# Optimization experiments

Hardware: AMD Instinct MI355X
Metric: run time of the kernel (lower is better)

Reference implementation:

```python
import jax, jax.numpy as jnp
import numpy as np

N, C, H, K = 4096, 512, 128, 3
NEG = -jnp.inf


def _linear(x, W, b):
    return x @ W.T + b


def _lrelu(x):
    return jnp.where(x > 0, x, 0.01 * x)  # nn.LeakyReLU default slope


def _cos_sim(x, y):
    # torch cal_cos_similarity: xy / (|x| |y|^T), NaN (0/0) -> 0
    xy = x @ y.T
    den = jnp.linalg.norm(x, axis=1, keepdims=True) * jnp.linalg.norm(y, axis=1, keepdims=True).T
    return xy / jnp.where(den == 0, 1.0, den)


def setup_inputs() -> dict:
    key = jax.random.key(0)
    ks = jax.random.split(key, 24)
    x_hidden = jax.random.normal(ks[0], (N, H), jnp.float32)
    cm = (jax.random.uniform(ks[1], (N, C)) < 0.05).astype(jnp.float32)
    # ensure every concept has at least one member stock (no empty concepts)
    cm = cm.at[jnp.arange(C) % N, jnp.arange(C)].set(1.0)
    market_value = jax.random.uniform(ks[2], (N,), jnp.float32, 0.1, 1.0)
    s = 1.0 / np.sqrt(H)
    inp = {"x_hidden": x_hidden, "concept_matrix": cm, "market_value": market_value}
    names = ["ps", "ps_fore", "ps_back", "hs", "hs_fore", "hs_back", "indi"]
    for i, n in enumerate(names):
        inp[f"W_{n}"] = jax.random.uniform(ks[3 + 2 * i], (H, H), jnp.float32, -s, s)
        inp[f"b_{n}"] = jax.random.uniform(ks[4 + 2 * i], (H,), jnp.float32, -s, s)
    inp["W_out"] = jax.random.uniform(ks[20], (1, H), jnp.float32, -s, s)
    inp["b_out"] = jax.random.uniform(ks[21], (1,), jnp.float32, -s, s)
    return inp


def reference(x_hidden, concept_matrix, market_value,
              W_ps, b_ps, W_ps_fore, b_ps_fore, W_ps_back, b_ps_back,
              W_hs, b_hs, W_hs_fore, b_hs_fore, W_hs_back, b_hs_back,
              W_indi, b_indi, W_out, b_out):
    x = x_hidden
    n = x.shape[0]
    # --- predefined-concept (ps) branch ---
    s2c = concept_matrix * market_value[:, None]                     # [N,C]
    s2c_den = s2c.sum(0)[None, :] * concept_matrix + 1.0
    s2c = s2c / s2c_den
    hidden = s2c.T @ x                                               # [C,H]
    valid1 = hidden.sum(1) != 0                                      # row-filter mask
    s2c2 = jax.nn.softmax(x @ hidden.T, axis=0)                      # softmax over stocks
    hidden = (s2c2.T @ x) * valid1[:, None]                          # [C,H]
    c2s = jax.nn.softmax(jnp.where(valid1[None, :], _cos_sim(x, hidden), NEG), axis=1)
    p_shared = _linear(c2s @ hidden, W_ps, b_ps)
    p_back = _linear(p_shared, W_ps_back, b_ps_back)
    out_ps = _lrelu(_linear(p_shared, W_ps_fore, b_ps_fore))
    # --- hidden-concept (hs) branch ---
    h = x - p_back
    hs2c = _cos_sim(h, h)                                            # [N,N]
    diag = jnp.diagonal(hs2c)
    hs2c = hs2c * (1.0 - jnp.eye(n, dtype=h.dtype))
    idx = jax.lax.top_k(hs2c, K)[1]                                  # [N,K]
    mask = jnp.zeros((n, n), h.dtype).at[jnp.arange(n)[:, None], idx].set(1.0)
    hs2c = hs2c * mask
    hs2c = hs2c + jnp.diag((hs2c.sum(0) != 0).astype(h.dtype) * diag)
    hidden2 = hs2c.T @ h                                             # [N,H]
    valid2 = hidden2.sum(1) != 0
    hidden2 = hidden2 * valid2[:, None]
    hc2s = jax.nn.softmax(jnp.where(valid2[None, :], _cos_sim(h, hidden2), NEG), axis=1)
    h_shared = _linear(hc2s @ hidden2, W_hs, b_hs)
    h_back = _linear(h_shared, W_hs_back, b_hs_back)
    out_hs = _lrelu(_linear(h_shared, W_hs_fore, b_hs_fore))
    # --- individual branch ---
    indiv = x - p_back - h_back
    out_indi = _lrelu(_linear(indiv, W_indi, b_indi))
    all_info = out_ps + out_hs + out_indi
    return _linear(all_info, W_out, b_out).squeeze()                 # [N]
```

## Files before the change

kernel.cpp:

```cpp
#include <hip/hip_runtime.h>
#include <hip/hip_fp16.h>
#include <math.h>

#define N 4096
#define C 512
#define H 128
#define PAD 40
#define WP 136
#define FWP 136
#define SP 136

typedef __attribute__((ext_vector_type(8))) short bf16x8;
typedef __attribute__((ext_vector_type(4))) float f32x4;


__device__ inline float wave_reduce_sum(float v) {
#pragma unroll
  for (int m = 32; m; m >>= 1) v += __shfl_xor(v, m);
  return v;
}

__device__ inline float lrelu(float v) { return v > 0.f ? v : 0.01f * v; }

__device__ inline bool better(float v, int j, float w, int k) {
// ... 94 lines not shown
               (unsigned)ll[12] | ((unsigned)ll[13] << 16), (unsigned)ll[14] | ((unsigned)ll[15] << 16)};
  *(uint4*)&thi[off] = ph0; *(uint4*)&thi[off + 8] = ph1;
  *(uint4*)&tlo[off] = pl0; *(uint4*)&tlo[off + 8] = pl1;
}


__global__ __launch_bounds__(64) void k_colsum_s2c(
    const float* __restrict__ cm, const float* __restrict__ mv,
    float* __restrict__ colsum_c) {
  int c = blockIdx.x * 64 + threadIdx.x;
  int i0 = blockIdx.y * 256;
  float acc = 0.f;
  for (int i = i0; i < i0 + 256; i++) acc += cm[(size_t)i * C + c] * mv[i];
  atomicAdd(&colsum_c[c], acc);
}

__global__ __launch_bounds__(256) void k_colstats(const float* __restrict__ sc,
                                                  float* __restrict__ colmax,
                                                  float* __restrict__ colsum) {
  __shared__ float red[256];
  int c = blockIdx.x, t = threadIdx.x;
  float v[16];
  float m = -3e38f;
#pragma unroll
  for (int q = 0; q < 16; q++) {
    v[q] = sc[(size_t)(q * 256 + t) * C + c];
    m = fmaxf(m, v[q]);
  }
  red[t] = m; __syncthreads();
  for (int s = 128; s; s >>= 1) { if (t < s) red[t] = fmaxf(red[t], red[t + s]); __syncthreads(); }
  m = red[0]; __syncthreads();
  float sum = 0.f;
#pragma unroll
  for (int q = 0; q < 16; q++) sum += __expf(v[q] - m);
  red[t] = sum; __syncthreads();
  for (int s = 128; s; s >>= 1) { if (t < s) red[t] += red[t + s]; __syncthreads(); }
  if (t == 0) { colmax[c] = m; colsum[c] = red[0]; }
}

__global__ __launch_bounds__(256) void k_cs_softmax(
    const float* __restrict__ sc, const float* __restrict__ xnorm,
    const float* __restrict__ hnorm, const float* __restrict__ valid1,
    unsigned short* __restrict__ cshi, unsigned short* __restrict__ cslo) {
  __shared__ float red[256];
  int i = blockIdx.x, t = threadIdx.x;
  float xn = xnorm[i];
  float r0 = sc[(size_t)i * C + t], r1 = sc[(size_t)i * C + 256 + t];
  float d0 = xn * hnorm[t], d1 = xn * hnorm[256 + t];
  float c0 = r0 / (d0 == 0.f ? 1.f : d0);
  float c1 = r1 / (d1 == 0.f ? 1.f : d1);
  float s0 = (valid1[t] != 0.f) ? c0 : -3e38f;
  float s1 = (valid1[256 + t] != 0.f) ? c1 : -3e38f;
  red[t] = fmaxf(s0, s1); __syncthreads();
  for (int s = 128; s; s >>= 1) { if (t < s) red[t] = fmaxf(red[t], red[t + s]); __syncthreads(); }
  float m = red[0]; __syncthreads();
  float p0 = (s0 > -1e37f) ? __expf(s0 - m) : 0.f;
  float p1 = (s1 > -1e37f) ? __expf(s1 - m) : 0.f;
  red[t] = p0 + p1; __syncthreads();
  for (int s = 128; s; s >>= 1) { if (t < s) red[t] += red[t + s]; __syncthreads(); }
  float inv = 1.f / red[0];
  float a = p0 * inv, b = p1 * inv;
  unsigned short ha = f2bf(a), hb = f2bf(b);
  cshi[(size_t)i * C + t] = ha;
  cslo[(size_t)i * C + t] = f2bf(a - bf2f(ha));
  cshi[(size_t)i * C + 256 + t] = hb;
  cslo[(size_t)i * C + 256 + t] = f2bf(b - bf2f(hb));
}

__global__ __launch_bounds__(64) void k_fin_hidden2(
    const float* __restrict__ h, const float* __restrict__ diagv,
    const float* __restrict__ colsum_m, float* __restrict__ hidden2,
    unsigned short* __restrict__ h2hi, unsigned short* __restrict__ h2lo,
    float* __restrict__ valid2f) {
  int j = blockIdx.x, t = threadIdx.x;
  float add = (colsum_m[j] != 0.f) ? diagv[j] : 0.f;
  float a = hidden2[(size_t)j * H + t] + add * h[(size_t)j * H + t];
  float b = hidden2[(size_t)j * H + 64 + t] + add * h[(size_t)j * H + 64 + t];
  float s = a + b, ss = a * a + b * b;
#pragma unroll
  for (int m = 32; m; m >>= 1) { s += __shfl_xor(s, m); ss += __shfl_xor(ss, m); }
  bool valid = (s != 0.f);
  a = valid ? a : 0.f; b = valid ? b : 0.f;
  hidden2[(size_t)j * H + t] = a;
  hidden2[(size_t)j * H + 64 + t] = b;
  float inv = (valid && ss > 0.f) ? (1.f / sqrtf(ss)) : 1.f;
  float va = a * inv, vb = b * inv;
  unsigned short ha = f2bf(va), hb = f2bf(vb);
  h2hi[(size_t)j * H + t] = ha;
  h2lo[(size_t)j * H + t] = f2bf(va - bf2f(ha));
  h2hi[(size_t)j * H + 64 + t] = hb;
  h2lo[(size_t)j * H + 64 + t] = f2bf(vb - bf2f(hb));
  if (t == 0) valid2f[j] = valid ? 1.f : 0.f;
}

__global__ __launch_bounds__(256) void k_mfma_nt(
    const unsigned short* __restrict__ Ahi, const unsigned short* __restrict__ Alo,
    const unsigned short* __restrict__ Bhi, const unsigned short* __restrict__ Blo,
    float* __restrict__ out, int Nn) {
  __shared__ __align__(16) unsigned short sAh[64 * PAD];
  __shared__ __align__(16) unsigned short sAl[64 * PAD];
  __shared__ __align__(16) unsigned short sBh[128 * PAD];
  __shared__ __align__(16) unsigned short sBl[128 * PAD];
  int tid = threadIdx.x;
  int bm = blockIdx.y * 64, bn = blockIdx.x * 128;
  int lane = tid & 63, w = tid >> 6;
  int wm = (w & 1) * 32, wn = (w >> 1) * 64;
  int l15 = lane & 15, quad = lane >> 4;
  f32x4 zero = {0.f, 0.f, 0.f, 0.f};
  f32x4 acc[2][4];
#pragma unroll
  for (int mt = 0; mt < 2; mt++)
#pragma unroll
    for (int nt = 0; nt < 4; nt++) acc[mt][nt] = zero;

  for (int kt = 0; kt < 128; kt += 32) {
    {
      int row = tid >> 2, ch = tid & 3;
      size_t ga = (size_t)(bm + row) * 128 + kt + ch * 8;
      int ls = row * PAD + ch * 8;
      *(uint4*)&sAh[ls] = *(const uint4*)&Ahi[ga];
      *(uint4*)&sAl[ls] = *(const uint4*)&Alo[ga];
    }
#pragma unroll
    for (int q = 0; q < 2; q++) {
      int f = q * 256 + tid;
      int row = f >> 2, ch = f & 3;
      size_t gb = (size_t)(bn + row) * 128 + kt + ch * 8;
      int ls = row * PAD + ch * 8;
      *(uint4*)&sBh[ls] = *(const uint4*)&Bhi[gb];
      *(uint4*)&sBl[ls] = *(const uint4*)&Blo[gb];
    }
    __syncthreads();
    bf16x8 ah[2], al[2], bh[4], bl[4];
#pragma unroll
    for (int t = 0; t < 2; t++) {
      int ar = (wm + t * 16 + l15) * PAD + quad * 8;
      ah[t] = *(const bf16x8*)&sAh[ar];
      al[t] = *(const bf16x8*)&sAl[ar];
    }
#pragma unroll
    for (int t = 0; t < 4; t++) {
      int br = (wn + t * 16 + l15) * PAD + quad * 8;
      bh[t] = *(const bf16x8*)&sBh[br];
      bl[t] = *(const bf16x8*)&sBl[br];
    }
#pragma unroll
    for (int mt = 0; mt < 2; mt++)
#pragma unroll
      for (int nt = 0; nt < 4; nt++) {
        acc[mt][nt] = __builtin_amdgcn_mfma_f32_16x16x32_bf16(ah[mt], bh[nt], acc[mt][nt], 0, 0, 0);
        acc[mt][nt] = __builtin_amdgcn_mfma_f32_16x16x32_bf16(ah[mt], bl[nt], acc[mt][nt], 0, 0, 0);
        acc[mt][nt] = __builtin_amdgcn_mfma_f32_16x16x32_bf16(al[mt], bh[nt], acc[mt][nt], 0, 0, 0);
      }
    __syncthreads();
  }
#pragma unroll
  for (int mt = 0; mt < 2; mt++) {
#pragma unroll
    for (int nt = 0; nt < 4; nt++) {
      int col = bn + wn + nt * 16 + l15;
#pragma unroll
      for (int rg = 0; rg < 4; rg++) {
        int row = bm + wm + mt * 16 + quad * 4 + rg;
        out[(size_t)row * Nn + col] = acc[mt][nt][rg];
      }
    }
  }
}

__global__ __launch_bounds__(512) void k_snt(
    const unsigned short* __restrict__ Ahi, const unsigned short* __restrict__ Alo,
    float2* __restrict__ cand) {
  __shared__ __align__(16) unsigned short sAh[128 * PAD];
  __shared__ __align__(16) unsigned short sAl[128 * PAD];
  __shared__ __align__(16) unsigned short sBh[128 * PAD];
  __shared__ __align__(16) unsigned short sBl[128 * PAD];
  __shared__ __align__(16) unsigned short sS[128 * SP];
  int tid = threadIdx.x;
  int bm = blockIdx.y * 128, bn = blockIdx.x * 128;
  int lane = tid & 63, w = tid >> 6;
  int wm = (w & 3) * 32, wn = (w >> 2) * 64;
  int l15 = lane & 15, quad = lane >> 4;
  f32x4 zero = {0.f, 0.f, 0.f, 0.f};
  f32x4 acc[2][4];
#pragma unroll
  for (int mt = 0; mt < 2; mt++)
#pragma unroll
    for (int nt = 0; nt < 4; nt++) acc[mt][nt] = zero;

  for (int kt = 0; kt < 128; kt += 32) {
    {
      int row = tid >> 2, ch = tid & 3;
      size_t ga = (size_t)(bm + row) * 128 + kt + ch * 8;
      size_t gb = (size_t)(bn + row) * 128 + kt + ch * 8;
      int ls = row * PAD + ch * 8;
      *(uint4*)&sAh[ls] = *(const uint4*)&Ahi[ga];
      *(uint4*)&sAl[ls] = *(const uint4*)&Alo[ga];
      *(uint4*)&sBh[ls] = *(const uint4*)&Ahi[gb];
      *(uint4*)&sBl[ls] = *(const uint4*)&Alo[gb];
    }
    __syncthreads();
    bf16x8 ah[2], al[2], bh[4], bl[4];
#pragma unroll
    for (int t = 0; t < 2; t++) {
      int ar = (wm + t * 16 + l15) * PAD + quad * 8;
      ah[t] = *(const bf16x8*)&sAh[ar];
      al[t] = *(const bf16x8*)&sAl[ar];
    }
#pragma unroll
    for (int t = 0; t < 4; t++) {
      int br = (wn + t * 16 + l15) * PAD + quad * 8;
      bh[t] = *(const bf16x8*)&sBh[br];
      bl[t] = *(const bf16x8*)&sBl[br];
    }
#pragma unroll
    for (int mt = 0; mt < 2; mt++)
#pragma unroll
      for (int nt = 0; nt < 4; nt++) {
        acc[mt][nt] = __builtin_amdgcn_mfma_f32_16x16x32_bf16(ah[mt], bh[nt], acc[mt][nt], 0, 0, 0);
        acc[mt][nt] = __builtin_amdgcn_mfma_f32_16x16x32_bf16(ah[mt], bl[nt], acc[mt][nt], 0, 0, 0);
        acc[mt][nt] = __builtin_amdgcn_mfma_f32_16x16x32_bf16(al[mt], bh[nt], acc[mt][nt], 0, 0, 0);
      }
    __syncthreads();
  }
#pragma unroll
  for (int mt = 0; mt < 2; mt++)
#pragma unroll
    for (int nt = 0; nt < 4; nt++) {
      int coll = wn + nt * 16 + l15;
#pragma unroll
      for (int rg = 0; rg < 4; rg++) {
        int rowl = wm + mt * 16 + quad * 4 + rg;
        float v = (bm + rowl == bn + coll) ? 0.f : acc[mt][nt][rg];
        sS[rowl * SP + coll] = __half_as_ushort(__float2half(v));
      }
    }
  __syncthreads();
  int r = tid >> 2, qf = tid & 3;
  const unsigned short* rowp = &sS[r * SP + qf * 32];
  int cbase = bn + qf * 32;
  float v5[5] = {-3e38f, -3e38f, -3e38f, -3e38f, -3e38f};
  int j5[5] = {0x7fffffff, 0x7fffffff, 0x7fffffff, 0x7fffffff, 0x7fffffff};
#pragma unroll
  for (int q = 0; q < 4; q++) {
    uint4 p = *(const uint4*)&rowp[q * 8];
    unsigned pk[4] = {p.x, p.y, p.z, p.w};
#pragma unroll
    for (int c2 = 0; c2 < 4; c2++) {
      float e0 = __half2float(__ushort_as_half((unsigned short)(pk[c2] & 0xffffu)));
      float e1 = __half2float(__ushort_as_half((unsigned short)(pk[c2] >> 16)));
      ins5(e0, cbase + q * 8 + c2 * 2, v5, j5);
      ins5(e1, cbase + q * 8 + c2 * 2 + 1, v5, j5);
    }
  }
  int slot = (bn >> 5) + qf;
  float2* cp = &cand[((size_t)(bm + r) * 128 + slot) * 5];
#pragma unroll
  for (int c2 = 0; c2 < 5; c2++) cp[c2] = {v5[c2], __int_as_float(j5[c2])};
}

__global__ __launch_bounds__(256) void k_rowtop2(
    const float2* __restrict__ cand, const float* __restrict__ hhat,
    float* __restrict__ mtv, int* __restrict__ mtj) {
  int i = blockIdx.x * 4 + (threadIdx.x >> 6);
  int lane = threadIdx.x & 63;
  const float2* cr = &cand[(size_t)i * 640];
  float v[5] = {-3e38f, -3e38f, -3e38f, -3e38f, -3e38f};
  int jx[5] = {0x7fffffff, 0x7fffffff, 0x7fffffff, 0x7fffffff, 0x7fffffff};
#pragma unroll
  for (int c = 0; c < 10; c++) {
    float2 p = cr[lane * 10 + c];
    ins5(p.x, __float_as_int(p.y), v, jx);
  }
#pragma unroll
  for (int d = 1; d < 64; d <<= 1) {
    float fv[5]; int fj[5];
#pragma unroll
    for (int c = 0; c < 5; c++) { fv[c] = __shfl_xor(v[c], d); fj[c] = __shfl_xor(jx[c], d); }
#pragma unroll
    for (int c = 0; c < 5; c++) ins5(fv[c], fj[c], v, jx);
  }
  const float* hi = &hhat[(size_t)i * H];
  float b0 = -3e38f, b1 = -3e38f, b2 = -3e38f;
  int q0 = 0, q1 = 0, q2 = 0;
#pragma unroll
  for (int c = 0; c < 5; c++) {
    int j = jx[c];
    float s;
    if (j == i) {
      s = 0.f;
    } else {
      const float* hj = &hhat[(size_t)j * H];
      float p = hi[lane] * hj[lane] + hi[lane + 64] * hj[lane + 64];
      s = wave_reduce_sum(p);
    }
    top3_ins(s, j, b0, q0, b1, q1, b2, q2);
  }
  if (lane == 0) {
    mtv[i * 3 + 0] = b0; mtv[i * 3 + 1] = b1; mtv[i * 3 + 2] = b2;
    mtj[i * 3 + 0] = q0; mtj[i * 3 + 1] = q1; mtj[i * 3 + 2] = q2;
  }
}

__global__ __launch_bounds__(256) void k_flash(
    const unsigned short* __restrict__ Qhi, const unsigned short* __restrict__ Qlo,
    const unsigned short* __restrict__ Khi, const unsigned short* __restrict__ Klo,
    const unsigned short* __restrict__ Vthi, const unsigned short* __restrict__ Vtlo,
    const float* __restrict__ valid2f, float* __restrict__ partialU,
    float* __restrict__ plsum, int KVC) {
  __shared__ __align__(16) unsigned short sQh[64 * FWP];
  __shared__ __align__(16) unsigned short sQl[64 * FWP];
  __shared__ __align__(16) unsigned short sP[64 * FWP];
  __shared__ __align__(16) unsigned short sKh[128 * PAD];
  __shared__ __align__(16) unsigned short sKl[128 * PAD];
  __shared__ float lsum_s[64];
  int tid = threadIdx.x;
  int z = blockIdx.x;
  int bm = blockIdx.y * 64;
  int j0 = z * KVC;
  int lane = tid & 63, w = tid >> 6;
  int wm = (w & 1) * 32, wn = (w >> 1) * 64;
  int l15 = lane & 15, quad = lane >> 4;
#pragma unroll
  for (int q = 0; q < 4; q++) {
    int f = q * 256 + tid;
    int row = f >> 4, ch = f & 15;
    size_t ga = (size_t)(bm + row) * 128 + ch * 8;
    int ls = row * FWP + ch * 8;
    *(uint4*)&sQh[ls] = *(const uint4*)&Qhi[ga];
    *(uint4*)&sQl[ls] = *(const uint4*)&Qlo[ga];
  }
  if (tid < 64) lsum_s[tid] = 0.f;
  __syncthreads();
  f32x4 zero = {0.f, 0.f, 0.f, 0.f};
  f32x4 uacc[2][4];
#pragma unroll
  for (int mt = 0; mt < 2; mt++)
#pragma unroll
    for (int nt = 0; nt < 4; nt++) uacc[mt][nt] = zero;

  for (int jb = j0; jb < j0 + KVC; jb += 128) {
    float vm[4];
#pragma unroll
    for (int nt = 0; nt < 4; nt++) vm[nt] = valid2f[jb + wn + nt * 16 + l15];
    f32x4 qacc[2][4];
#pragma unroll
    for (int mt = 0; mt < 2; mt++)
#pragma unroll
      for (int nt = 0; nt < 4; nt++) qacc[mt][nt] = zero;
    for (int kt = 0; kt < 128; kt += 32) {
#pragma unroll
      for (int q = 0; q < 2; q++) {
        int f = q * 256 + tid;
        int row = f >> 2, ch = f & 3;
        size_t gb = (size_t)(jb + row) * 128 + kt + ch * 8;
        int ls = row * PAD + ch * 8;
        *(uint4*)&sKh[ls] = *(const uint4*)&Khi[gb];
        *(uint4*)&sKl[ls] = *(const uint4*)&Klo[gb];
      }
      __syncthreads();
      bf16x8 ah[2], al[2], bh[4], bl[4];
#pragma unroll
      for (int t = 0; t < 2; t++) {
        int ar = (wm + t * 16 + l15) * FWP + kt + quad * 8;
        ah[t] = *(const bf16x8*)&sQh[ar];
        al[t] = *(const bf16x8*)&sQl[ar];
      }
#pragma unroll
      for (int t = 0; t < 4; t++) {
        int br = (wn + t * 16 + l15) * PAD + quad * 8;
        bh[t] = *(const bf16x8*)&sKh[br];
        bl[t] = *(const bf16x8*)&sKl[br];
      }
#pragma unroll
      for (int mt = 0; mt < 2; mt++)
#pragma unroll
        for (int nt = 0; nt < 4; nt++) {
          qacc[mt][nt] = __builtin_amdgcn_mfma_f32_16x16x32_bf16(ah[mt], bh[nt], qacc[mt][nt], 0, 0, 0);
          qacc[mt][nt] = __builtin_amdgcn_mfma_f32_16x16x32_bf16(ah[mt], bl[nt], qacc[mt][nt], 0, 0, 0);
          qacc[mt][nt] = __builtin_amdgcn_mfma_f32_16x16x32_bf16(al[mt], bh[nt], qacc[mt][nt], 0, 0, 0);
        }
      __syncthreads();
    }
#pragma unroll
    for (int mt = 0; mt < 2; mt++) {
#pragma unroll
      for (int rg = 0; rg < 4; rg++) {
        int row = wm + mt * 16 + quad * 4 + rg;
        float rs = 0.f;
#pragma unroll
        for (int nt = 0; nt < 4; nt++) {
          float e = (vm[nt] != 0.f) ? __expf(qacc[mt][nt][rg] - 1.f) : 0.f;
          rs += e;
          sP[row * FWP + wn + nt * 16 + l15] = f2bf(e);
        }
#pragma unroll
        for (int d = 1; d < 16; d <<= 1) rs += __shfl_xor(rs, d);
        if (l15 == 0) atomicAdd(&lsum_s[row], rs);
      }
    }
    __syncthreads();
    for (int kt = 0; kt < 128; kt += 32) {
      bf16x8 pa[2], vh[4], vl[4];
#pragma unroll
      for (int t = 0; t < 2; t++) {
        int ar = (wm + t * 16 + l15) * FWP + kt + quad * 8;
        pa[t] = *(const bf16x8*)&sP[ar];
      }
#pragma unroll
      for (int t = 0; t < 4; t++) {
        size_t gv = (size_t)(wn + t * 16 + l15) * N + jb + kt + quad * 8;
        vh[t] = *(const bf16x8*)&Vthi[gv];
        vl[t] = *(const bf16x8*)&Vtlo[gv];
      }
#pragma unroll
      for (int mt = 0; mt < 2; mt++)
#pragma unroll
        for (int nt = 0; nt < 4; nt++) {
          uacc[mt][nt] = __builtin_amdgcn_mfma_f32_16x16x32_bf16(pa[mt], vh[nt], uacc[mt][nt], 0, 0, 0);
          uacc[mt][nt] = __builtin_amdgcn_mfma_f32_16x16x32_bf16(pa[mt], vl[nt], uacc[mt][nt], 0, 0, 0);
        }
    }
  }
  float* pU = partialU + (size_t)z * N * 128;
#pragma unroll
  for (int mt = 0; mt < 2; mt++)
#pragma unroll
    for (int nt = 0; nt < 4; nt++) {
      int col = wn + nt * 16 + l15;
#pragma unroll
      for (int rg = 0; rg < 4; rg++) {
        int row = bm + wm + mt * 16 + quad * 4 + rg;
        pU[(size_t)row * 128 + col] = uacc[mt][nt][rg];
      }
    }
  __syncthreads();
  if (tid < 64) plsum[(size_t)z * N + bm + tid] = lsum_s[tid];
}

__global__ __launch_bounds__(256) void k_mfma_kn(
    const unsigned short* __restrict__ Ahi, const unsigned short* __restrict__ Alo,
    const unsigned short* __restrict__ Bthi, const unsigned short* __restrict__ Btlo,
    float* __restrict__ partial, int lda, int KC) {
  __shared__ __align__(16) unsigned short sAh[128 * PAD];
  __shared__ __align__(16) unsigned short sAl[128 * PAD];
  __shared__ __align__(16) unsigned short sBh[128 * PAD];
  __shared__ __align__(16) unsigned short sBl[128 * PAD];
  int tid = threadIdx.x;
  int bm = blockIdx.y * 128;
  int k0 = blockIdx.z * KC;
  int lane = tid & 63, w = tid >> 6;
  int wm = (w & 1) * 64, wn = (w >> 1) * 64;
  int l15 = lane & 15, quad = lane >> 4;
  f32x4 zero = {0.f, 0.f, 0.f, 0.f};
  f32x4 acc[4][4];
#pragma unroll
  for (int mt = 0; mt < 4; mt++)
#pragma unroll
    for (int nt = 0; nt < 4; nt++) acc[mt][nt] = zero;

  for (int kt = 0; kt < KC; kt += 32) {
#pragma unroll
    for (int q = 0; q < 2; q++) {
      int f = tid * 2 + q;
      int row = f >> 2, ch = f & 3;
      size_t ga = (size_t)(bm + row) * lda + k0 + kt + ch * 8;
      size_t gb = (size_t)row * lda + k0 + kt + ch * 8;
      int ls = row * PAD + ch * 8;
      *(uint4*)&sAh[ls] = *(const uint4*)&Ahi[ga];
      *(uint4*)&sAl[ls] = *(const uint4*)&Alo[ga];
      *(uint4*)&sBh[ls] = *(const uint4*)&Bthi[gb];
      *(uint4*)&sBl[ls] = *(const uint4*)&Btlo[gb];
    }
    __syncthreads();
    bf16x8 ah[4], al[4], bh[4], bl[4];
#pragma unroll
    for (int t = 0; t < 4; t++) {
      int ar = (wm + t * 16 + l15) * PAD + quad * 8;
      ah[t] = *(const bf16x8*)&sAh[ar];
      al[t] = *(const bf16x8*)&sAl[ar];
      int br = (wn + t * 16 + l15) * PAD + quad * 8;
      bh[t] = *(const bf16x8*)&sBh[br];
      bl[t] = *(const bf16x8*)&sBl[br];
    }
#pragma unroll
    for (int mt = 0; mt < 4; mt++)
#pragma unroll
      for (int nt = 0; nt < 4; nt++) {
        acc[mt][nt] = __builtin_amdgcn_mfma_f32_16x16x32_bf16(ah[mt], bh[nt], acc[mt][nt], 0, 0, 0);
        acc[mt][nt] = __builtin_amdgcn_mfma_f32_16x16x32_bf16(ah[mt], bl[nt], acc[mt][nt], 0, 0, 0);
        acc[mt][nt] = __builtin_amdgcn_mfma_f32_16x16x32_bf16(al[mt], bh[nt], acc[mt][nt], 0, 0, 0);
      }
    __syncthreads();
  }
  float* pp = partial + (size_t)blockIdx.z * N * 128;
#pragma unroll
  for (int mt = 0; mt < 4; mt++)
#pragma unroll
    for (int nt = 0; nt < 4; nt++) {
      int col = wn + nt * 16 + l15;
#pragma unroll
      for (int rg = 0; rg < 4; rg++) {
        int row = bm + wm + mt * 16 + quad * 4 + rg;
        pp[(size_t)row * 128 + col] = acc[mt][nt][rg];
      }
    }
}

template <int AMODE>
__global__ __launch_bounds__(256) void k_mfma_genA(
    const float* __restrict__ P, const float* __restrict__ mv,
    const float* __restrict__ col1, const float* __restrict__ col2,
    const unsigned short* __restrict__ Bthi, const unsigned short* __restrict__ Btlo,
    float* __restrict__ partial, int KC) {
  __shared__ __align__(16) unsigned short sAh[128 * PAD];
  __shared__ __align__(16) unsigned short sAl[128 * PAD];
  __shared__ __align__(16) unsigned short sBh[128 * PAD];
  __shared__ __align__(16) unsigned short sBl[128 * PAD];
  int tid = threadIdx.x;
  int bm = blockIdx.y * 128;
  int k0 = blockIdx.z * KC;
  int lane = tid & 63, w = tid >> 6;
  int wm = (w & 1) * 64, wn = (w >> 1) * 64;
  int l15 = lane & 15, quad = lane >> 4;
  f32x4 zero = {0.f, 0.f, 0.f, 0.f};
  f32x4 acc[4][4];
#pragma unroll
  for (int mt = 0; mt < 4; mt++)
#pragma unroll
    for (int nt = 0; nt < 4; nt++) acc[mt][nt] = zero;

  for (int kt = 0; kt < KC; kt += 32) {
    int kr = tid >> 3;
    int mc = (tid & 7) * 16;
    int k = k0 + kt + kr;
    float mvk = (AMODE == 1) ? mv[k] : 0.f;
#pragma unroll
    for (int q = 0; q < 4; q++) {
      int m0 = mc + q * 4;
      float4 pv = *(const float4*)&P[(size_t)k * C + bm + m0];
      float4 c1 = *(const float4*)&col1[bm + m0];
      float wv[4];
      if (AMODE == 1) {
        wv[0] = pv.x * mvk / (c1.x * pv.x + 1.f);
        wv[1] = pv.y * mvk / (c1.y * pv.y + 1.f);
        wv[2] = pv.z * mvk / (c1.z * pv.z + 1.f);
        wv[3] = pv.w * mvk / (c1.w * pv.w + 1.f);
      } else {
        float4 c2 = *(const float4*)&col2[bm + m0];
        wv[0] = __expf(pv.x - c1.x) / c2.x;
        wv[1] = __expf(pv.y - c1.y) / c2.y;
        wv[2] = __expf(pv.z - c1.z) / c2.z;
        wv[3] = __expf(pv.w - c1.w) / c2.w;
      }
#pragma unroll
      for (int j = 0; j < 4; j++) {
        unsigned short hh = f2bf(wv[j]);
        sAh[(m0 + j) * PAD + kr] = hh;
        sAl[(m0 + j) * PAD + kr] = f2bf(wv[j] - bf2f(hh));
      }
    }
#pragma unroll
    for (int q = 0; q < 2; q++) {
      int f = q * 256 + tid;
      int row = f >> 2, ch = f & 3;
      size_t gb = (size_t)row * N + k0 + kt + ch * 8;
      int ls = row * PAD + ch * 8;
      *(uint4*)&sBh[ls] = *(const uint4*)&Bthi[gb];
      *(uint4*)&sBl[ls] = *(const uint4*)&Btlo[gb];
    }
    __syncthreads();
    bf16x8 ah[4], al[4], bh[4], bl[4];
#pragma unroll
    for (int t = 0; t < 4; t++) {
      int ar = (wm + t * 16 + l15) * PAD + quad * 8;
      ah[t] = *(const bf16x8*)&sAh[ar];
      al[t] = *(const bf16x8*)&sAl[ar];
      int br = (wn + t * 16 + l15) * PAD + quad * 8;
      bh[t] = *(const bf16x8*)&sBh[br];
      bl[t] = *(const bf16x8*)&sBl[br];
    }
#pragma unroll
    for (int mt = 0; mt < 4; mt++)
#pragma unroll
      for (int nt = 0; nt < 4; nt++) {
        acc[mt][nt] = __builtin_amdgcn_mfma_f32_16x16x32_bf16(ah[mt], bh[nt], acc[mt][nt], 0, 0, 0);
        acc[mt][nt] = __builtin_amdgcn_mfma_f32_16x16x32_bf16(ah[mt], bl[nt], acc[mt][nt], 0, 0, 0);
        acc[mt][nt] = __builtin_amdgcn_mfma_f32_16x16x32_bf16(al[mt], bh[nt], acc[mt][nt], 0, 0, 0);
      }
    __syncthreads();
  }
  float* pp = partial + (size_t)blockIdx.z * C * 128;
#pragma unroll
  for (int mt = 0; mt < 4; mt++)
#pragma unroll
    for (int nt = 0; nt < 4; nt++) {
      int col = wn + nt * 16 + l15;
#pragma unroll
      for (int rg = 0; rg < 4; rg++) {
        int row = bm + wm + mt * 16 + quad * 4 + rg;
        pp[(size_t)row * 128 + col] = acc[mt][nt][rg];
      }
    }
}

__global__ __launch_bounds__(256) void k_scatter(
    const float* __restrict__ mtv, const int* __restrict__ mtj,
    const float* __restrict__ h, float* __restrict__ hidden2,
    float* __restrict__ colsum_m) {
  int i = blockIdx.x * 4 + (threadIdx.x >> 6);
  int lane = threadIdx.x & 63;
  float h0 = h[(size_t)i * H + lane], h1 = h[(size_t)i * H + 64 + lane];
#pragma unroll
  for (int s = 0; s < 3; s++) {
    float v = mtv[i * 3 + s];
    int j = mtj[i * 3 + s];
    atomicAdd(&hidden2[(size_t)j * H + lane], v * h0);
    atomicAdd(&hidden2[(size_t)j * H + 64 + lane], v * h1);
    if (lane == s) atomicAdd(&colsum_m[j], v);
  }
}

__global__ __launch_bounds__(256) void k_reduce(
    const float* __restrict__ partial, float* __restrict__ out, int cnt,
    size_t slot, size_t size4, const float* __restrict__ scalem,
    const float* __restrict__ plsum, unsigned short* __restrict__ hi,
    unsigned short* __restrict__ lo, float* __restrict__ nrmout,
    float* __restrict__ validout) {
  size_t idx = (size_t)blockIdx.x * 256 + threadIdx.x;
  if (idx >= size4) return;
  float4 s = {0, 0, 0, 0};
  for (int c = 0; c < cnt; c++) {
    float4 v = *(const float4*)&partial[c * slot + idx * 4];
    s.x += v.x; s.y += v.y; s.z += v.z; s.w += v.w;
  }
  if (scalem) {
    float sc = scalem[idx >> 5];
    s.x *= sc; s.y *= sc; s.z *= sc; s.w *= sc;
  }
  if (plsum) {
    int r = idx >> 5;
    float d = 0.f;
    for (int c = 0; c < cnt; c++) d += plsum[(size_t)c * N + r];
    float sc = 1.f / d;
    s.x *= sc; s.y *= sc; s.z *= sc; s.w *= sc;
  }
  *(float4*)&out[idx * 4] = s;
  if (hi) {
    float vv[4] = {s.x, s.y, s.z, s.w};
    unsigned short h[4], l[4];
#pragma unroll
    for (int c = 0; c < 4; c++) {
      h[c] = f2bf(vv[c]);
      l[c] = f2bf(vv[c] - bf2f(h[c]));
    }
    uint2 ph = {(unsigned)h[0] | ((unsigned)h[1] << 16),
                (unsigned)h[2] | ((unsigned)h[3] << 16)};
    uint2 pl = {(unsigned)l[0] | ((unsigned)l[1] << 16),
                (unsigned)l[2] | ((unsigned)l[3] << 16)};
    *(uint2*)&hi[idx * 4] = ph;
    *(uint2*)&lo[idx * 4] = pl;
  }
  if (nrmout || validout) {
    float rs = s.x + s.y + s.z + s.w;
    float rq = s.x * s.x + s.y * s.y + s.z * s.z + s.w * s.w;
#pragma unroll
    for (int m = 16; m; m >>= 1) { rs += __shfl_xor(rs, m); rq += __shfl_xor(rq, m); }
    if ((threadIdx.x & 31) == 0) {
      if (nrmout) nrmout[idx >> 5] = sqrtf(rq);
      if (validout) validout[idx >> 5] = (rs != 0.f) ? 1.f : 0.f;
    }
  }
}


#define LOAD_W(Wt)                                                        \
  do {                                                                    \
    _Pragma("unroll") for (int q = 0; q < 16; q++) {                      \
      int f = q * 256 + tid;                                              \
      int wr = f >> 5, wc = (f & 31) * 4;                                 \
      float4 wv = *(const float4*)&(Wt)[(size_t)wr * 128 + wc];           \
      float ww[4] = {wv.x, wv.y, wv.z, wv.w};                             \
      _Pragma("unroll") for (int c = 0; c < 4; c++) {                     \
        unsigned short hh = f2bf(ww[c]);                                  \
        sWh[wr * WP + wc + c] = hh;                                       \
        sWl[wr * WP + wc + c] = f2bf(ww[c] - bf2f(hh));                   \
      }                                                                   \
    }                                                                     \
  } while (0)

#define GEMM32(accv)                                                              \
  do {                                                                            \
    _Pragma("unroll") for (int nt = 0; nt < 4; nt++) accv[nt] = zero;             \
    _Pragma("unroll") for (int kt = 0; kt < 128; kt += 32) {                      \
      bf16x8 ah = *(const bf16x8*)&sAh[(rt + l15) * WP + kt + quad * 8];          \
      bf16x8 al = *(const bf16x8*)&sAl[(rt + l15) * WP + kt + quad * 8];          \
      _Pragma("unroll") for (int nt = 0; nt < 4; nt++) {                          \
        int br = (ch2 + nt * 16 + l15) * WP + kt + quad * 8;                      \
        bf16x8 bh = *(const bf16x8*)&sWh[br];                                     \
        bf16x8 bl = *(const bf16x8*)&sWl[br];                                     \
        accv[nt] = __builtin_amdgcn_mfma_f32_16x16x32_bf16(ah, bh, accv[nt], 0, 0, 0); \
        accv[nt] = __builtin_amdgcn_mfma_f32_16x16x32_bf16(ah, bl, accv[nt], 0, 0, 0); \
        accv[nt] = __builtin_amdgcn_mfma_f32_16x16x32_bf16(al, bh, accv[nt], 0, 0, 0); \
      }                                                                           \
    }                                                                             \
  } while (0)

__global__ __launch_bounds__(256) void k_ps_tail(
    const float* __restrict__ A, const float* __restrict__ x,
    const float* __restrict__ W_ps, const float* __restrict__ b_ps,
    const float* __restrict__ W_psb, const float* __restrict__ b_psb,
    const float* __restrict__ W_psf, const float* __restrict__ b_psf,
    float* __restrict__ hbuf, float* __restrict__ hhat,
    unsigned short* __restrict__ hhi, unsigned short* __restrict__ hlo,
    float* __restrict__ diagv, float* __restrict__ all_info) {
  __shared__ __align__(16) unsigned short sWh[128 * WP];
  __shared__ __align__(16) unsigned short sWl[128 * WP];
  __shared__ __align__(16) unsigned short sAh[32 * WP];
  __shared__ __align__(16) unsigned short sAl[32 * WP];
  __shared__ __align__(16) float sF[32][132];
  int tid = threadIdx.x;
  int bm = blockIdx.x * 32;
  int lane = tid & 63, w = tid >> 6;
  int rt = (w & 1) * 16, ch2 = (w >> 1) * 64;
  int l15 = lane & 15, quad = lane >> 4;
  f32x4 zero = {0.f, 0.f, 0.f, 0.f};
  f32x4 acc[4];

  {
    int row = tid >> 3, c0 = (tid & 7) * 16;
    const float* src = &A[(size_t)(bm + row) * 128 + c0];
#pragma unroll
    for (int q = 0; q < 4; q++) {
      float4 v = *(const float4*)&src[q * 4];
      float vv[4] = {v.x, v.y, v.z, v.w};
#pragma unroll
      for (int c = 0; c < 4; c++) {
        unsigned short hh = f2bf(vv[c]);
        sAh[row * WP + c0 + q * 4 + c] = hh;
        sAl[row * WP + c0 + q * 4 + c] = f2bf(vv[c] - bf2f(hh));
      }
    }
  }
  LOAD_W(W_ps);
  __syncthreads();
  GEMM32(acc);
  __syncthreads();
#pragma unroll
  for (int nt = 0; nt < 4; nt++) {
    int col = ch2 + nt * 16 + l15;
    float bv = b_ps[col];
#pragma unroll
    for (int rg = 0; rg < 4; rg++) {
      int row = rt + quad * 4 + rg;
      float v = acc[nt][rg] + bv;
      unsigned short hh = f2bf(v);
      sAh[row * WP + col] = hh;
      sAl[row * WP + col] = f2bf(v - bf2f(hh));
    }
  }
  LOAD_W(W_psb);
  __syncthreads();
  GEMM32(acc);
#pragma unroll
  for (int nt = 0; nt < 4; nt++) {
    int col = ch2 + nt * 16 + l15;
    float bv = b_psb[col];
#pragma unroll
    for (int rg = 0; rg < 4; rg++) {
      int row = rt + quad * 4 + rg;
      size_t off = (size_t)(bm + row) * 128 + col;
      float hv = x[off] - (acc[nt][rg] + bv);
      hbuf[off] = hv;
      sF[row][col] = hv;
    }
  }
  __syncthreads();
  {
    int row = tid >> 3, c0 = (tid & 7) * 16;
    float hv16[16];
    float ssp = 0.f;
#pragma unroll
    for (int q = 0; q < 16; q++) {
      float v = sF[row][c0 + q];
      hv16[q] = v;
      ssp += v * v;
    }
    ssp += __shfl_xor(ssp, 1);
    ssp += __shfl_xor(ssp, 2);
    ssp += __shfl_xor(ssp, 4);
    float ss = ssp;
    float hn = sqrtf(ss);
    float den = hn * hn;
    float dg = (den == 0.f) ? 0.f : ss / den;
    float inv = (ss > 0.f) ? (1.f / hn) : 1.f;
    size_t base = (size_t)(bm + row) * H + c0;
    float va16[16];
    unsigned short hh16[16], ll16[16];
#pragma unroll
    for (int q = 0; q < 16; q++) {
      va16[q] = hv16[q] * inv;
      hh16[q] = f2bf(va16[q]);
      ll16[q] = f2bf(va16[q] - bf2f(hh16[q]));
    }
#pragma unroll
    for (int q4 = 0; q4 < 4; q4++) {
      float4 fv = {va16[q4 * 4], va16[q4 * 4 + 1], va16[q4 * 4 + 2], va16[q4 * 4 + 3]};
      *(float4*)&hhat[base + q4 * 4] = fv;
    }
    uint4 ph0 = {(unsigned)hh16[0] | ((unsigned)hh16[1] << 16), (unsigned)hh16[2] | ((unsigned)hh16[3] << 16),
                 (unsigned)hh16[4] | ((unsigned)hh16[5] << 16), (unsigned)hh16[6] | ((unsigned)hh16[7] << 16)};
    uint4 ph1 = {(unsigned)hh16[8] | ((unsigned)hh16[9] << 16), (unsigned)hh16[10] | ((unsigned)hh16[11] << 16),
                 (unsigned)hh16[12] | ((unsigned)hh16[13] << 16), (unsigned)hh16[14] | ((unsigned)hh16[15] << 16)};
    uint4 pl0 = {(unsigned)ll16[0] | ((unsigned)ll16[1] << 16), (unsigned)ll16[2] | ((unsigned)ll16[3] << 16),
                 (unsigned)ll16[4] | ((unsigned)ll16[5] << 16), (unsigned)ll16[6] | ((unsigned)ll16[7] << 16)};
    uint4 pl1 = {(unsigned)ll16[8] | ((unsigned)ll16[9] << 16), (unsigned)ll16[10] | ((unsigned)ll16[11] << 16),
                 (unsigned)ll16[12] | ((unsigned)ll16[13] << 16), (unsigned)ll16[14] | ((unsigned)ll16[15] << 16)};
    *(uint4*)&hhi[base] = ph0; *(uint4*)&hhi[base + 8] = ph1;
    *(uint4*)&hlo[base] = pl0; *(uint4*)&hlo[base + 8] = pl1;
    if ((tid & 7) == 0) diagv[bm + row] = dg;
  }
  LOAD_W(W_psf);
  __syncthreads();
  GEMM32(acc);
#pragma unroll
  for (int nt = 0; nt < 4; nt++) {
    int col = ch2 + nt * 16 + l15;
    float bv = b_psf[col];
#pragma unroll
    for (int rg = 0; rg < 4; rg++) {
      int row = rt + quad * 4 + rg;
      size_t off = (size_t)(bm + row) * 128 + col;
      all_info[off] = lrelu(acc[nt][rg] + bv);
    }
  }
}

__global__ __launch_bounds__(256) void k_hs_tail(
    const float* __restrict__ A, const float* __restrict__ hbuf,
    const float* __restrict__ all_info,
    const float* __restrict__ W_hs, const float* __restrict__ b_hs,
    const float* __restrict__ W_hsf, const float* __restrict__ b_hsf,
    const float* __restrict__ W_hsb, const float* __restrict__ b_hsb,
    const float* __restrict__ W_in, const float* __restrict__ b_in,
    const float* __restrict__ W_out, const float* __restrict__ b_out,
    float* __restrict__ out) {
  __shared__ __align__(16) unsigned short sWh[128 * WP];
  __shared__ __align__(16) unsigned short sWl[128 * WP];
  __shared__ __align__(16) unsigned short sAh[32 * WP];
  __shared__ __align__(16) unsigned short sAl[32 * WP];
  __shared__ __align__(16) float sF[32][132];
  int tid = threadIdx.x;
  int bm = blockIdx.x * 32;
  int lane = tid & 63, w = tid >> 6;
  int rt = (w & 1) * 16, ch2 = (w >> 1) * 64;
  int l15 = lane & 15, quad = lane >> 4;
  f32x4 zero = {0.f, 0.f, 0.f, 0.f};
  f32x4 acc[4];
  float allv[4][4];

  {
    int row = tid >> 3, c0 = (tid & 7) * 16;
    const float* src = &A[(size_t)(bm + row) * 128 + c0];
#pragma unroll
    for (int q = 0; q < 4; q++) {
      float4 v = *(const float4*)&src[q * 4];
      float vv[4] = {v.x, v.y, v.z, v.w};
#pragma unroll
      for (int c = 0; c < 4; c++) {
        unsigned short hh = f2bf(vv[c]);
        sAh[row * WP + c0 + q * 4 + c] = hh;
        sAl[row * WP + c0 + q * 4 + c] = f2bf(vv[c] - bf2f(hh));
      }
    }
  }
  LOAD_W(W_hs);
  __syncthreads();
  GEMM32(acc);
  __syncthreads();
#pragma unroll
  for (int nt = 0; nt < 4; nt++) {
    int col = ch2 + nt * 16 + l15;
    float bv = b_hs[col];
#pragma unroll
    for (int rg = 0; rg < 4; rg++) {
      int row = rt + quad * 4 + rg;
      float v = acc[nt][rg] + bv;
      unsigned short hh = f2bf(v);
      sAh[row * WP + col] = hh;
      sAl[row * WP + col] = f2bf(v - bf2f(hh));
    }
  }
  LOAD_W(W_hsf);
  __syncthreads();
  GEMM32(acc);
#pragma unroll
  for (int nt = 0; nt < 4; nt++) {
    int col = ch2 + nt * 16 + l15;
    float bv = b_hsf[col];
#pragma unroll
    for (int rg = 0; rg < 4; rg++) {
      int row = rt + quad * 4 + rg;
      size_t off = (size_t)(bm + row) * 128 + col;
      allv[nt][rg] = all_info[off] + lrelu(acc[nt][rg] + bv);
    }
  }
  __syncthreads();
  LOAD_W(W_hsb);
  __syncthreads();
  GEMM32(acc);
  float iv[4][4];
#pragma unroll
  for (int nt = 0; nt < 4; nt++) {
    int col = ch2 + nt * 16 + l15;
    float bv = b_hsb[col];
#pragma unroll
    for (int rg = 0; rg < 4; rg++) {
      int row = rt + quad * 4 + rg;
      size_t off = (size_t)(bm + row) * 128 + col;
      iv[nt][rg] = hbuf[off] - (acc[nt][rg] + bv);
    }
  }
  __syncthreads();
#pragma unroll
  for (int nt = 0; nt < 4; nt++) {
    int col = ch2 + nt * 16 + l15;
#pragma unroll
    for (int rg = 0; rg < 4; rg++) {
      int row = rt + quad * 4 + rg;
      unsigned short hh = f2bf(iv[nt][rg]);
      sAh[row * WP + col] = hh;
      sAl[row * WP + col] = f2bf(iv[nt][rg] - bf2f(hh));
    }
  }
  LOAD_W(W_in);
  __syncthreads();
  GEMM32(acc);
#pragma unroll
  for (int nt = 0; nt < 4; nt++) {
    int col = ch2 + nt * 16 + l15;
    float bv = b_in[col];
#pragma unroll
    for (int rg = 0; rg < 4; rg++) {
      int row = rt + quad * 4 + rg;
      allv[nt][rg] += lrelu(acc[nt][rg] + bv);
      sF[row][col] = allv[nt][rg];
    }
  }
  __syncthreads();
  {
    int row = tid >> 3, c0 = (tid & 7) * 16;
    float s = 0.f;
#pragma unroll
    for (int q = 0; q < 16; q++) s += sF[row][c0 + q] * W_out[c0 + q];
    s += __shfl_xor(s, 1);
    s += __shfl_xor(s, 2);
    s += __shfl_xor(s, 4);
    if ((tid & 7) == 0) out[bm + row] = s + b_out[0];
  }
}


extern "C" void kernel_launch(void* const* d_in, const int* in_sizes, int n_in,
                              void* d_out, int out_size, void* d_ws, size_t ws_size,
                              hipStream_t stream) {
  (void)in_sizes; (void)n_in; (void)out_size; (void)ws_size;
  const float* x   = (const float*)d_in[0];
  const float* cm  = (const float*)d_in[1];
  const float* mv  = (const float*)d_in[2];
  const float* W_ps = (const float*)d_in[3],  *b_ps = (const float*)d_in[4];
  const float* W_psf = (const float*)d_in[5], *b_psf = (const float*)d_in[6];
  const float* W_psb = (const float*)d_in[7], *b_psb = (const float*)d_in[8];
  const float* W_hs = (const float*)d_in[9],  *b_hs = (const float*)d_in[10];
  const float* W_hsf = (const float*)d_in[11], *b_hsf = (const float*)d_in[12];
  const float* W_hsb = (const float*)d_in[13], *b_hsb = (const float*)d_in[14];
  const float* W_in = (const float*)d_in[15], *b_in = (const float*)d_in[16];
  const float* W_out = (const float*)d_in[17], *b_out = (const float*)d_in[18];
  float* out = (float*)d_out;

  float* W = (float*)d_ws;
  size_t o = 0;
  auto alloc = [&](size_t n) { float* p = W + o; o += n; return p; };
  float* colsum_c = alloc(C);
  float* colmax   = alloc(C);
  float* colsumexp= alloc(C);
  float* valid1   = alloc(C);
  float* hnorm_ps = alloc(C);
  float* xnorm    = alloc(N);
  float* diagv    = alloc(N);
  float* colsum_m = alloc(N);
  float* valid2f  = alloc(N);
  float* plsum    = alloc((size_t)8 * N);
  float* mtv      = alloc(3 * N);
  int*   mtj      = (int*)alloc(3 * N);
  float* hidden1  = alloc((size_t)C * H);
  float* hidden_ps= alloc((size_t)C * H);
  float* scores   = alloc((size_t)N * C);
  float* ps_pre   = alloc((size_t)N * H);
  float* all_info = alloc((size_t)N * H);
  float* hbuf     = alloc((size_t)N * H);
  float* hhat     = alloc((size_t)N * H);
  float* hidden2  = alloc((size_t)N * H);
  unsigned short* xhi    = (unsigned short*)alloc((size_t)N * H / 2);
  unsigned short* xlo    = (unsigned short*)alloc((size_t)N * H / 2);
  unsigned short* hhathi = (unsigned short*)alloc((size_t)N * H / 2);
  unsigned short* hhatlo = (unsigned short*)alloc((size_t)N * H / 2);
  unsigned short* h2hi   = (unsigned short*)alloc((size_t)N * H / 2);
  unsigned short* h2lo   = (unsigned short*)alloc((size_t)N * H / 2);
  unsigned short* h1hi   = (unsigned short*)alloc((size_t)C * H / 2);
  unsigned short* h1lo   = (unsigned short*)alloc((size_t)C * H / 2);
  unsigned short* hpshi  = (unsigned short*)alloc((size_t)C * H / 2);
  unsigned short* hpslo  = (unsigned short*)alloc((size_t)C * H / 2);
  unsigned short* cshi   = (unsigned short*)alloc((size_t)N * C / 2);
  unsigned short* cslo   = (unsigned short*)alloc((size_t)N * C / 2);
  unsigned short* hpst_hi= (unsigned short*)alloc((size_t)H * C / 2);
  unsigned short* hpst_lo= (unsigned short*)alloc((size_t)H * C / 2);
  unsigned short* h2t_hi = (unsigned short*)alloc((size_t)H * N / 2);
  unsigned short* h2t_lo = (unsigned short*)alloc((size_t)H * N / 2);
  unsigned short* xt_hi  = (unsigned short*)alloc((size_t)H * N / 2);
  unsigned short* xt_lo  = (unsigned short*)alloc((size_t)H * N / 2);
  float2* cand    = (float2*)alloc((size_t)N * 128 * 5 * 2);
  float* partial  = W + o;
  const int Z = 8;
  const int ZG = 64;

  hipMemsetAsync(colsum_c, 0, C * sizeof(float), stream);
  hipMemsetAsync(colsum_m, 0, N * sizeof(float), stream);
  hipMemsetAsync(hidden2, 0, (size_t)N * H * sizeof(float), stream);

  dim3 blk(256);
  k_split<<<dim3(N * H / 1024), blk, 0, stream>>>(x, xhi, xlo, xnorm);
  k_tsplit<<<dim3(N / 32), blk, 0, stream>>>(x, xt_hi, xt_lo, N);
  k_colsum_s2c<<<dim3(C / 64, 16), dim3(64), 0, stream>>>(cm, mv, colsum_c);
  k_mfma_genA<1><<<dim3(1, C / 128, ZG), blk, 0, stream>>>(
      cm, mv, colsum_c, nullptr, xt_hi, xt_lo, partial, N / ZG);
  k_reduce<<<dim3(C * H / 4 / 256), blk, 0, stream>>>(
      partial, hidden1, ZG, (size_t)C * H, (size_t)C * H / 4, nullptr, nullptr,
      h1hi, h1lo, nullptr, valid1);
  k_mfma_nt<<<dim3(C / 128, N / 64), blk, 0, stream>>>(
      xhi, xlo, h1hi, h1lo, scores, C);
  k_colstats<<<dim3(C), blk, 0, stream>>>(scores, colmax, colsumexp);
  k_mfma_genA<2><<<dim3(1, C / 128, ZG), blk, 0, stream>>>(
      scores, nullptr, colmax, colsumexp, xt_hi, xt_lo, partial, N / ZG);
  k_reduce<<<dim3(C * H / 4 / 256), blk, 0, stream>>>(
      partial, hidden_ps, ZG, (size_t)C * H, (size_t)C * H / 4, valid1, nullptr,
      hpshi, hpslo, hnorm_ps, nullptr);
  k_mfma_nt<<<dim3(C / 128, N / 64), blk, 0, stream>>>(
      xhi, xlo, hpshi, hpslo, scores, C);
  k_cs_softmax<<<dim3(N), blk, 0, stream>>>(scores, xnorm, hnorm_ps, valid1,
                                            cshi, cslo);
  k_tsplit<<<dim3(C / 32), blk, 0, stream>>>(hidden_ps, hpst_hi, hpst_lo, C);
  k_mfma_kn<<<dim3(1, N / 128, 4), blk, 0, stream>>>(
      cshi, cslo, hpst_hi, hpst_lo, partial, C, C / 4);
  k_reduce<<<dim3(N * H / 4 / 256), blk, 0, stream>>>(
      partial, ps_pre, 4, (size_t)N * H, (size_t)N * H / 4, nullptr, nullptr,
      nullptr, nullptr, nullptr, nullptr);
  k_ps_tail<<<dim3(N / 32), blk, 0, stream>>>(
      ps_pre, x, W_ps, b_ps, W_psb, b_psb, W_psf, b_psf,
      hbuf, hhat, hhathi, hhatlo, diagv, all_info);
  k_snt<<<dim3(N / 128, N / 128), dim3(512), 0, stream>>>(
      hhathi, hhatlo, cand);
  k_rowtop2<<<dim3(N / 4), blk, 0, stream>>>(cand, hhat, mtv, mtj);
  k_scatter<<<dim3(N / 4), blk, 0, stream>>>(mtv, mtj, hbuf, hidden2, colsum_m);
  k_fin_hidden2<<<dim3(N), dim3(64), 0, stream>>>(hbuf, diagv, colsum_m, hidden2,
                                                  h2hi, h2lo, valid2f);
  k_tsplit<<<dim3(N / 32), blk, 0, stream>>>(hidden2, h2t_hi, h2t_lo, N);
  k_flash<<<dim3(Z, N / 64), blk, 0, stream>>>(
      hhathi, hhatlo, h2hi, h2lo, h2t_hi, h2t_lo, valid2f, partial, plsum,
      N / Z);
  k_reduce<<<dim3(N * H / 4 / 256), blk, 0, stream>>>(
      partial, ps_pre, Z, (size_t)N * H, (size_t)N * H / 4, nullptr, plsum,
      nullptr, nullptr, nullptr, nullptr);
  k_hs_tail<<<dim3(N / 32), blk, 0, stream>>>(
      ps_pre, hbuf, all_info, W_hs, b_hs, W_hsf, b_hsf, W_hsb, b_hsb,
      W_in, b_in, W_out, b_out, out);
}
```

Measured before the change: 385.0 us.

## Double-buffer K/V tiles in flash kernel with 512-thread 128-row blocks

The flash-style hidden-concept attention kernel now uses 512 threads covering 128 query rows per block. It stages K and V^T tiles through a double-buffered LDS ring, prefetching the next tile into registers while the current MFMAs run. Previously V was read straight from global memory inside the PV loop. This is meant to hide load latency and reuse the K/V tiles across more query rows, at the cost of more LDS and registers per block and fewer blocks. Separately, the split-K factor for the k_mfma_kn GEMM goes from 4 to 8 for more parallelism, which adds reduction work.

```diff
diff --git a/kernel.cpp b/kernel.cpp
--- a/kernel.cpp
+++ b/kernel.cpp
@@ -420,36 +420,47 @@
   }
 }
 
-__global__ __launch_bounds__(256) void k_flash(
+__global__ __launch_bounds__(512) void k_flash(
     const unsigned short* __restrict__ Qhi, const unsigned short* __restrict__ Qlo,
     const unsigned short* __restrict__ Khi, const unsigned short* __restrict__ Klo,
     const unsigned short* __restrict__ Vthi, const unsigned short* __restrict__ Vtlo,
     const float* __restrict__ valid2f, float* __restrict__ partialU,
     float* __restrict__ plsum, int KVC) {
-  __shared__ __align__(16) unsigned short sQh[64 * FWP];
-  __shared__ __align__(16) unsigned short sQl[64 * FWP];
-  __shared__ __align__(16) unsigned short sP[64 * FWP];
-  __shared__ __align__(16) unsigned short sKh[128 * PAD];
-  __shared__ __align__(16) unsigned short sKl[128 * PAD];
-  __shared__ float lsum_s[64];
+  __shared__ __align__(16) unsigned short sQh[128 * FWP];
+  __shared__ __align__(16) unsigned short sQl[128 * FWP];
+  __shared__ __align__(16) unsigned short sP[128 * FWP];
+  __shared__ __align__(16) unsigned short sBh[2][128 * PAD];
+  __shared__ __align__(16) unsigned short sBl[2][128 * PAD];
+  __shared__ float lsum_s[128];
   int tid = threadIdx.x;
   int z = blockIdx.x;
-  int bm = blockIdx.y * 64;
+  int bm = blockIdx.y * 128;
   int j0 = z * KVC;
   int lane = tid & 63, w = tid >> 6;
-  int wm = (w & 1) * 32, wn = (w >> 1) * 64;
+  int wm = (w & 3) * 32, wn = (w >> 2) * 64;
   int l15 = lane & 15, quad = lane >> 4;
+  int srow = tid >> 2, sch = tid & 3;
+  int sls = srow * PAD + sch * 8;
 #pragma unroll
   for (int q = 0; q < 4; q++) {
-    int f = q * 256 + tid;
+    int f = q * 512 + tid;
     int row = f >> 4, ch = f & 15;
     size_t ga = (size_t)(bm + row) * 128 + ch * 8;
     int ls = row * FWP + ch * 8;
     *(uint4*)&sQh[ls] = *(const uint4*)&Qhi[ga];
     *(uint4*)&sQl[ls] = *(const uint4*)&Qlo[ga];
   }
-  if (tid < 64) lsum_s[tid] = 0.f;
-  __syncthreads();
+  if (tid < 128) lsum_s[tid] = 0.f;
+  {
+    size_t a = (size_t)(j0 + srow) * 128 + sch * 8;
+    uint4 rh = *(const uint4*)&Khi[a];
+    uint4 rl = *(const uint4*)&Klo[a];
+    __syncthreads();
+    *(uint4*)&sBh[0][sls] = rh;
+    *(uint4*)&sBl[0][sls] = rl;
+  }
+  __syncthreads();
+  int cur = 0;
   f32x4 zero = {0.f, 0.f, 0.f, 0.f};
   f32x4 uacc[2][4];
 #pragma unroll
@@ -466,29 +477,31 @@
     for (int mt = 0; mt < 2; mt++)
 #pragma unroll
       for (int nt = 0; nt < 4; nt++) qacc[mt][nt] = zero;
-    for (int kt = 0; kt < 128; kt += 32) {
-#pragma unroll
-      for (int q = 0; q < 2; q++) {
-        int f = q * 256 + tid;
-        int row = f >> 2, ch = f & 3;
-        size_t gb = (size_t)(jb + row) * 128 + kt + ch * 8;
-        int ls = row * PAD + ch * 8;
-        *(uint4*)&sKh[ls] = *(const uint4*)&Khi[gb];
-        *(uint4*)&sKl[ls] = *(const uint4*)&Klo[gb];
-      }
-      __syncthreads();
+#pragma unroll
+    for (int t = 0; t < 4; t++) {
+      uint4 nrh, nrl;
+      if (t < 3) {
+        size_t a = (size_t)(jb + srow) * 128 + (t + 1) * 32 + sch * 8;
+        nrh = *(const uint4*)&Khi[a];
+        nrl = *(const uint4*)&Klo[a];
+      } else {
+        size_t a = (size_t)srow * N + jb + sch * 8;
+        nrh = *(const uint4*)&Vthi[a];
+        nrl = *(const uint4*)&Vtlo[a];
+      }
+      int kt = t * 32;
       bf16x8 ah[2], al[2], bh[4], bl[4];
 #pragma unroll
-      for (int t = 0; t < 2; t++) {
-        int ar = (wm + t * 16 + l15) * FWP + kt + quad * 8;
-        ah[t] = *(const bf16x8*)&sQh[ar];
-        al[t] = *(const bf16x8*)&sQl[ar];
-      }
-#pragma unroll
-      for (int t = 0; t < 4; t++) {
-        int br = (wn + t * 16 + l15) * PAD + quad * 8;
-        bh[t] = *(const bf16x8*)&sKh[br];
-        bl[t] = *(const bf16x8*)&sKl[br];
+      for (int tt = 0; tt < 2; tt++) {
+        int ar = (wm + tt * 16 + l15) * FWP + kt + quad * 8;
+        ah[tt] = *(const bf16x8*)&sQh[ar];
+        al[tt] = *(const bf16x8*)&sQl[ar];
+      }
+#pragma unroll
+      for (int tt = 0; tt < 4; tt++) {
+        int br = (wn + tt * 16 + l15) * PAD + quad * 8;
+        bh[tt] = *(const bf16x8*)&sBh[cur][br];
+        bl[tt] = *(const bf16x8*)&sBl[cur][br];
       }
 #pragma unroll
       for (int mt = 0; mt < 2; mt++)
@@ -498,7 +511,10 @@
           qacc[mt][nt] = __builtin_amdgcn_mfma_f32_16x16x32_bf16(ah[mt], bl[nt], qacc[mt][nt], 0, 0, 0);
           qacc[mt][nt] = __builtin_amdgcn_mfma_f32_16x16x32_bf16(al[mt], bh[nt], qacc[mt][nt], 0, 0, 0);
         }
+      *(uint4*)&sBh[cur ^ 1][sls] = nrh;
+      *(uint4*)&sBl[cur ^ 1][sls] = nrl;
       __syncthreads();
+      cur ^= 1;
     }
 #pragma unroll
     for (int mt = 0; mt < 2; mt++) {
@@ -518,18 +534,35 @@
       }
     }
     __syncthreads();
-    for (int kt = 0; kt < 128; kt += 32) {
+#pragma unroll
+    for (int t = 0; t < 4; t++) {
+      uint4 nrh = {0, 0, 0, 0}, nrl = {0, 0, 0, 0};
+      bool have;
+      if (t < 3) {
+        have = true;
+        size_t a = (size_t)srow * N + jb + (t + 1) * 32 + sch * 8;
+        nrh = *(const uint4*)&Vthi[a];
+        nrl = *(const uint4*)&Vtlo[a];
+      } else {
+        have = (jb + 128 < j0 + KVC);
+        if (have) {
+          size_t a = (size_t)(jb + 128 + srow) * 128 + sch * 8;
+          nrh = *(const uint4*)&Khi[a];
+          nrl = *(const uint4*)&Klo[a];
+        }
+      }
+      int kt = t * 32;
       bf16x8 pa[2], vh[4], vl[4];
 #pragma unroll
-      for (int t = 0; t < 2; t++) {
-        int ar = (wm + t * 16 + l15) * FWP + kt + quad * 8;
-        pa[t] = *(const bf16x8*)&sP[ar];
-      }
-#pragma unroll
-      for (int t = 0; t < 4; t++) {
-        size_t gv = (size_t)(wn + t * 16 + l15) * N + jb + kt + quad * 8;
-        vh[t] = *(const bf16x8*)&Vthi[gv];
-        vl[t] = *(const bf16x8*)&Vtlo[gv];
+      for (int tt = 0; tt < 2; tt++) {
+        int ar = (wm + tt * 16 + l15) * FWP + kt + quad * 8;
+        pa[tt] = *(const bf16x8*)&sP[ar];
+      }
+#pragma unroll
+      for (int tt = 0; tt < 4; tt++) {
+        int br = (wn + tt * 16 + l15) * PAD + quad * 8;
+        vh[tt] = *(const bf16x8*)&sBh[cur][br];
+        vl[tt] = *(const bf16x8*)&sBl[cur][br];
       }
 #pragma unroll
       for (int mt = 0; mt < 2; mt++)
@@ -538,6 +571,12 @@
           uacc[mt][nt] = __builtin_amdgcn_mfma_f32_16x16x32_bf16(pa[mt], vh[nt], uacc[mt][nt], 0, 0, 0);
           uacc[mt][nt] = __builtin_amdgcn_mfma_f32_16x16x32_bf16(pa[mt], vl[nt], uacc[mt][nt], 0, 0, 0);
         }
+      if (have) {
+        *(uint4*)&sBh[cur ^ 1][sls] = nrh;
+        *(uint4*)&sBl[cur ^ 1][sls] = nrl;
+      }
+      __syncthreads();
+      cur ^= 1;
     }
   }
   float* pU = partialU + (size_t)z * N * 128;
@@ -552,8 +591,7 @@
         pU[(size_t)row * 128 + col] = uacc[mt][nt][rg];
       }
     }
-  __syncthreads();
-  if (tid < 64) plsum[(size_t)z * N + bm + tid] = lsum_s[tid];
+  if (tid < 128) plsum[(size_t)z * N + bm + tid] = lsum_s[tid];
 }
 
 __global__ __launch_bounds__(256) void k_mfma_kn(
@@ -1141,6 +1179,7 @@
   float* partial  = W + o;
   const int Z = 8;
   const int ZG = 64;
+  const int ZK = 8;
 
   hipMemsetAsync(colsum_c, 0, C * sizeof(float), stream);
   hipMemsetAsync(colsum_m, 0, N * sizeof(float), stream);
@@ -1168,10 +1207,10 @@
   k_cs_softmax<<<dim3(N), blk, 0, stream>>>(scores, xnorm, hnorm_ps, valid1,
                                             cshi, cslo);
   k_tsplit<<<dim3(C / 32), blk, 0, stream>>>(hidden_ps, hpst_hi, hpst_lo, C);
-  k_mfma_kn<<<dim3(1, N / 128, 4), blk, 0, stream>>>(
-      cshi, cslo, hpst_hi, hpst_lo, partial, C, C / 4);
+  k_mfma_kn<<<dim3(1, N / 128, ZK), blk, 0, stream>>>(
+      cshi, cslo, hpst_hi, hpst_lo, partial, C, C / ZK);
   k_reduce<<<dim3(N * H / 4 / 256), blk, 0, stream>>>(
-      partial, ps_pre, 4, (size_t)N * H, (size_t)N * H / 4, nullptr, nullptr,
+      partial, ps_pre, ZK, (size_t)N * H, (size_t)N * H / 4, nullptr, nullptr,
       nullptr, nullptr, nullptr, nullptr);
   k_ps_tail<<<dim3(N / 32), blk, 0, stream>>>(
       ps_pre, x, W_ps, b_ps, W_psb, b_psb, W_psf, b_psf,
@@ -1183,7 +1222,7 @@
   k_fin_hidden2<<<dim3(N), dim3(64), 0, stream>>>(hbuf, diagv, colsum_m, hidden2,
                                                   h2hi, h2lo, valid2f);
   k_tsplit<<<dim3(N / 32), blk, 0, stream>>>(hidden2, h2t_hi, h2t_lo, N);
-  k_flash<<<dim3(Z, N / 64), blk, 0, stream>>>(
+  k_flash<<<dim3(Z, N / 128), dim3(512), 0, stream>>>(
       hhathi, hhatlo, h2hi, h2lo, h2t_hi, h2t_lo, valid2f, partial, plsum,
       N / Z);
   k_reduce<<<dim3(N * H / 4 / 256), blk, 0, stream>>>(
```

Measured after the change: 369.2 us. 1.04x faster.
